# Kernel optimization log

Measured on AMD Instinct MI355X. Metric: run time of the kernel, lower is better.

Reference implementation:

```python
import jax, jax.numpy as jnp
import numpy as np

# --- static config (mirrors init_kwargs) ---
B, N, CBEV = 4, 4, 64
D, FH, FW = 41, 16, 44          # depth bins, feature H/W after downsample
OGH, OGW, DS = 256, 704, 16     # original image dims, downsample
NX, NY, NZ = 240, 240, 1        # BEV grid (x, y, z)
DX = np.array([0.4, 0.4, 20.0], np.float32)            # voxel size
BX = np.array([-47.8, -47.8, 0.0], np.float32)          # voxel grid origin (bound+dx/2)


def _frustum():
    # [D, FH, FW, 3] with (u_pixel, v_pixel, depth); UD discretization 4..44 step 1
    ds = (4.0 + np.arange(D, dtype=np.float32)).reshape(D, 1, 1) * np.ones((1, FH, FW), np.float32)
    xs = np.linspace(0.0, OGW - 1, FW, dtype=np.float32).reshape(1, 1, FW) * np.ones((D, FH, 1), np.float32)
    ys = np.linspace(0.0, OGH - 1, FH, dtype=np.float32).reshape(1, FH, 1) * np.ones((D, 1, FW), np.float32)
    return jnp.asarray(np.stack([xs, ys, ds], axis=-1))


def setup_inputs() -> dict:
    key = jax.random.key(0)
    x = jax.random.normal(key, (B, N, D, FH, FW, CBEV), dtype=jnp.float32)
    # realistic camera rig: 4 cameras at yaw 0/90/180/270 deg, pinhole intrinsics
    intr = np.zeros((N, 3, 3), np.float32)
    rot = np.zeros((N, 3, 3), np.float32)
    tr = np.zeros((N, 3), np.float32)
    cam2ego = np.array([[0, 0, 1], [-1, 0, 0], [0, -1, 0]], np.float32)  # cam z-fwd -> ego x-fwd
    for n in range(N):
        intr[n] = np.array([[500.0, 0.0, OGW / 2.0], [0.0, 500.0, OGH / 2.0], [0.0, 0.0, 1.0]], np.float32)
        yaw = 2.0 * np.pi * n / N
        c, s = np.cos(yaw), np.sin(yaw)
        Rz = np.array([[c, -s, 0], [s, c, 0], [0, 0, 1]], np.float32)
        rot[n] = Rz @ cam2ego
        tr[n] = np.array([1.5 * c, 1.5 * s, 1.6], np.float32)
    rots = jnp.asarray(np.broadcast_to(rot, (B, N, 3, 3)).copy())
    trans = jnp.asarray(np.broadcast_to(tr, (B, N, 3)).copy())
    intrins = jnp.asarray(np.broadcast_to(intr, (B, N, 3, 3)).copy())
    post_rots = jnp.asarray(np.broadcast_to(np.eye(3, dtype=np.float32), (B, N, 3, 3)).copy())
    post_trans = jnp.zeros((B, N, 3), jnp.float32)
    return {"x": x, "rots": rots, "trans": trans, "intrins": intrins,
            "post_rots": post_rots, "post_trans": post_trans}


def reference(x, rots, trans, intrins, post_rots, post_trans):
    # --- get_geometry: frustum pixel/depth points -> ego-frame xyz ---
    frustum = _frustum()                                            # [D,FH,FW,3]
    pts = frustum[None, None] - post_trans[:, :, None, None, None, :]
    pts = jnp.einsum('bnij,bndhwj->bndhwi', jnp.linalg.inv(post_rots), pts)
    pts = jnp.concatenate([pts[..., :2] * pts[..., 2:3], pts[..., 2:3]], axis=-1)
    combine = rots @ jnp.linalg.inv(intrins)
    pts = jnp.einsum('bnij,bndhwj->bndhwi', combine, pts) + trans[:, :, None, None, None, :]
    # --- voxel_pooling: quantize, mask OOB, segment-sum into dense BEV grid ---
    dx = jnp.asarray(DX)
    bx = jnp.asarray(BX)
    vox = ((pts - (bx - dx / 2.0)) / dx).astype(jnp.int32)          # trunc, same as torch .long()
    vx, vy, vz = vox[..., 0], vox[..., 1], vox[..., 2]              # [B,N,D,FH,FW]
    kept = (vx >= 0) & (vx < NX) & (vy >= 0) & (vy < NY) & (vz >= 0) & (vz < NZ)
    bidx = jnp.arange(B, dtype=jnp.int32)[:, None, None, None, None]
    nvox = B * NZ * NY * NX
    lin = bidx * (NZ * NY * NX) + vz * (NY * NX) + vy * NX + vx
    lin = jnp.where(kept, lin, nvox).reshape(-1)                    # invalid -> dummy bin
    feats = x.reshape(-1, CBEV)                                     # [Nprime, C]
    sums = jax.ops.segment_sum(feats, lin, num_segments=nvox + 1)[:nvox]
    final = sums.reshape(B, NZ, NY, NX, CBEV).transpose(0, 1, 4, 2, 3)  # [B,Z,C,Y,X]
    # torch: cat(final.unbind(dim=2), 1) on [B,C,Z,Y,X] -> [B, Z*C, Y, X] z-major
    return final.reshape(B, NZ * CBEV, NY, NX)
```

## Files before the change

### kernel.cpp

```cpp
#include <hip/hip_runtime.h>

#define BB   4
#define NNC  4
#define DDEP 41
#define FHH  16
#define FWW  44
#define CC   64
#define NXX  240
#define NYY  240
#define NVOX (BB*NYY*NXX)
#define NTRI (BB*NNC*DDEP*FWW)
#define SLOTS 8

#define W_CNT  0
#define W_TAB  (NVOX*4)
#define W_VSUM (W_TAB + NVOX*SLOTS*4)

__device__ __forceinline__ void inv3x3_upper_f32(const float K[9], float o[9]) {
    float a00 = __fdiv_rn(1.0f, K[0]);
    float a11 = __fdiv_rn(1.0f, K[4]);
    float a22 = __fdiv_rn(1.0f, K[8]);
    float b01 = __fmul_rn(-a11, __fmul_rn(a00, K[1]));
    float x0 = __fadd_rn(__fmul_rn(a00, K[2]), __fmul_rn(b01, K[5]));
    float x1 = __fmul_rn(a11, K[5]);
    float b02 = __fmul_rn(-a22, x0);
    float b12 = __fmul_rn(-a22, x1);
    o[0]=a00; o[1]=b01; o[2]=b02;
    o[3]=0.0f; o[4]=a11; o[5]=b12;
    o[6]=0.0f; o[7]=0.0f; o[8]=a22;
}

__global__ void __launch_bounds__(256) megageom(
        const float* __restrict__ x,
        const float* __restrict__ rots,
        const float* __restrict__ trans,
        const float* __restrict__ intrins,
        const float* __restrict__ post_rots,
        const float* __restrict__ post_trans,
        int* __restrict__ cnt,
        int* __restrict__ table,
        float* __restrict__ vsum) {
    int tri  = blockIdx.x*4 + (threadIdx.x >> 6);
    int lane = threadIdx.x & 63;
    if (tri >= NTRI) return;

    int w  = tri % FWW;
    int d  = (tri / FWW) % DDEP;
    int bn = tri / (FWW*DDEP);

    float K[9], PR[9], R[9];
    #pragma unroll
    for (int i = 0; i < 9; ++i) {
        K[i]  = intrins[bn*9 + i];
        PR[i] = post_rots[bn*9 + i];
        R[i]  = rots[bn*9 + i];
    }
    float Ki[9], PRi[9];
    inv3x3_upper_f32(K, Ki);
    inv3x3_upper_f32(PR, PRi);
    float C[9];
    #pragma unroll
    for (int i = 0; i < 3; ++i)
        #pragma unroll
        for (int j = 0; j < 3; ++j) {
            float s = __fmul_rn(R[i*3+0], Ki[0*3+j]);
            s = __fadd_rn(s, __fmul_rn(R[i*3+1], Ki[1*3+j]));
            s = __fadd_rn(s, __fmul_rn(R[i*3+2], Ki[2*3+j]));
            C[i*3+j] = s;
        }
    float ptx = post_trans[bn*3+0], pty = post_trans[bn*3+1], ptz = post_trans[bn*3+2];
    float trx = trans[bn*3+0], try_ = trans[bn*3+1], trz = trans[bn*3+2];

    int h = lane & 15;
    float u  = (float)((double)w * (703.0/43.0));
    float v  = (float)((double)h * 17.0);
    float dd = (float)(4 + d);

    float p0x = __fsub_rn(u,  ptx);
    float p0y = __fsub_rn(v,  pty);
    float p0z = __fsub_rn(dd, ptz);
    float p1x = __fadd_rn(__fadd_rn(__fmul_rn(PRi[0],p0x), __fmul_rn(PRi[1],p0y)), __fmul_rn(PRi[2],p0z));
    float p1y = __fadd_rn(__fadd_rn(__fmul_rn(PRi[3],p0x), __fmul_rn(PRi[4],p0y)), __fmul_rn(PRi[5],p0z));
    float p1z = __fadd_rn(__fadd_rn(__fmul_rn(PRi[6],p0x), __fmul_rn(PRi[7],p0y)), __fmul_rn(PRi[8],p0z));
    float p2x = __fmul_rn(p1x, p1z);
    float p2y = __fmul_rn(p1y, p1z);
    float p2z = p1z;
    float ex = __fadd_rn(__fadd_rn(__fmul_rn(C[0],p2x), __fmul_rn(C[1],p2y)), __fmul_rn(C[2],p2z));
    float ey = __fadd_rn(__fadd_rn(__fmul_rn(C[3],p2x), __fmul_rn(C[4],p2y)), __fmul_rn(C[5],p2z));
    float ez = __fadd_rn(__fadd_rn(__fmul_rn(C[6],p2x), __fmul_rn(C[7],p2y)), __fmul_rn(C[8],p2z));
    float gx = __fadd_rn(ex, trx);
    float gy = __fadd_rn(ey, try_);
    float gz = __fadd_rn(ez, trz);

    float qx = __fdiv_rn(__fsub_rn(gx, -48.0f), 0.4f);
    float qy = __fdiv_rn(__fsub_rn(gy, -48.0f), 0.4f);
    float qz = __fdiv_rn(__fsub_rn(gz, -10.0f), 20.0f);
    int vx = (int)qx;
    int vy = (int)qy;
    int vz = (int)qz;

    bool kept = (vx >= 0) & (vx < NXX) & (vy >= 0) & (vy < NYY) & (vz == 0) & (lane < 16);
    unsigned int mask = (unsigned int)(__ballot(kept) & 0xFFFFull);
    if (mask == 0) return;

    const float* xb = x + (size_t)((bn*DDEP + d)*FHH*FWW + w)*CC + lane;
    float a[8];
    #pragma unroll
    for (int k = 0; k < 8; ++k) a[k] = 0.0f;
    #pragma unroll
    for (int hh = 0; hh < 16; ++hh)
        if ((mask >> hh) & 1) a[hh & 7] += xb[(size_t)hh*(FWW*CC)];
    #pragma unroll
    for (int k = 0; k < 4; ++k) a[k] += a[k + 4];
    vsum[(size_t)tri*CC + lane] = (a[0] + a[1]) + (a[2] + a[3]);

    if (lane == 0) {
        int b  = bn / NNC;
        int vb = b*(NYY*NXX) + vy*NXX + vx;
        int sl = atomicAdd(&cnt[vb], 1);
        if (sl < SLOTS) table[vb*SLOTS + sl] = tri;
    }
}

__global__ void __launch_bounds__(256) assemble(
        const int* __restrict__ cnt,
        const int* __restrict__ table,
        const float* __restrict__ vsum,
        float* __restrict__ out) {
    __shared__ float lds[16*65];
    int tid  = threadIdx.x;
    int wid  = tid >> 6;
    int lane = tid & 63;
    int v0   = blockIdx.x*16;

    #pragma unroll
    for (int k = 0; k < 4; ++k) {
        int cell = v0 + wid*4 + k;
        int n = cnt[cell]; if (n > SLOTS) n = SLOTS;
        const int* tp = table + cell*SLOTS;
        int tt = (lane < n) ? tp[lane] : 0;
        float s0 = 0.0f, s1 = 0.0f, s2 = 0.0f, s3 = 0.0f;
        int i = 0;
        for (; i + 4 <= n; i += 4) {
            int t0 = __shfl(tt, i+0), t1 = __shfl(tt, i+1);
            int t2 = __shfl(tt, i+2), t3 = __shfl(tt, i+3);
            s0 += vsum[(size_t)t0*CC + lane];
            s1 += vsum[(size_t)t1*CC + lane];
            s2 += vsum[(size_t)t2*CC + lane];
            s3 += vsum[(size_t)t3*CC + lane];
        }
        for (; i < n; ++i) s0 += vsum[(size_t)__shfl(tt, i)*CC + lane];
        lds[(wid*4 + k)*65 + lane] = (s0 + s1) + (s2 + s3);
    }
    __syncthreads();

    int c = tid >> 2, q = tid & 3;
    float4 f;
    f.x = lds[(q*4 + 0)*65 + c];
    f.y = lds[(q*4 + 1)*65 + c];
    f.z = lds[(q*4 + 2)*65 + c];
    f.w = lds[(q*4 + 3)*65 + c];
    int b  = v0 / (NYY*NXX);
    int yx = v0 % (NYY*NXX);
    *(float4*)&out[(size_t)b*(CC*NYY*NXX) + (size_t)c*(NYY*NXX) + yx + q*4] = f;
}

extern "C" void kernel_launch(void* const* d_in, const int* in_sizes, int n_in,
                              void* d_out, int out_size, void* d_ws, size_t ws_size,
                              hipStream_t stream) {
    const float* x          = (const float*)d_in[0];
    const float* rots       = (const float*)d_in[1];
    const float* trans      = (const float*)d_in[2];
    const float* intrins    = (const float*)d_in[3];
    const float* post_rots  = (const float*)d_in[4];
    const float* post_trans = (const float*)d_in[5];
    float* out = (float*)d_out;

    char* ws = (char*)d_ws;
    int*   cnt   = (int*)(ws + W_CNT);
    int*   table = (int*)(ws + W_TAB);
    float* vsum  = (float*)(ws + W_VSUM);

    hipMemsetAsync(cnt, 0, NVOX*sizeof(int), stream);
    megageom<<<(NTRI + 3)/4, 256, 0, stream>>>(x, rots, trans, intrins,
                                               post_rots, post_trans,
                                               cnt, table, vsum);
    assemble<<<NVOX/16, 256, 0, stream>>>(cnt, table, vsum, out);
}
```

Measured before the change: 243.1 us.

## Defer feature gathering to assemble and pack counters and table entries

The geometry kernel no longer reads features or writes per-triple partial sums. It only records (triple index, 16-bit height mask) entries in the per-cell table, and it packs per-cell counters into bytes so the memset shrinks fourfold. The assemble kernel now gathers the masked x rows directly, which removes the vsum write and reread round trip. Each geometry wavefront now handles four triples at 16 lanes each. In exchange, the feature gathers move into the assemble pass, with data-dependent loops over mask bits, and the byte counters could overflow if more than 255 triples hit one cell.

```diff
diff --git a/kernel.cpp b/kernel.cpp
--- a/kernel.cpp
+++ b/kernel.cpp
@@ -13,8 +13,7 @@
 #define SLOTS 8
 
 #define W_CNT  0
-#define W_TAB  (NVOX*4)
-#define W_VSUM (W_TAB + NVOX*SLOTS*4)
+#define W_TAB  (NVOX)
 
 __device__ __forceinline__ void inv3x3_upper_f32(const float K[9], float o[9]) {
     float a00 = __fdiv_rn(1.0f, K[0]);
@@ -30,23 +29,24 @@
     o[6]=0.0f; o[7]=0.0f; o[8]=a22;
 }
 
-__global__ void __launch_bounds__(256) megageom(
-        const float* __restrict__ x,
+__global__ void __launch_bounds__(256) geom(
         const float* __restrict__ rots,
         const float* __restrict__ trans,
         const float* __restrict__ intrins,
         const float* __restrict__ post_rots,
         const float* __restrict__ post_trans,
-        int* __restrict__ cnt,
-        int* __restrict__ table,
-        float* __restrict__ vsum) {
-    int tri  = blockIdx.x*4 + (threadIdx.x >> 6);
+        unsigned int* __restrict__ cntp,
+        unsigned int* __restrict__ table) {
+    int wid  = threadIdx.x >> 6;
     int lane = threadIdx.x & 63;
-    if (tri >= NTRI) return;
+    int sub  = lane >> 4;
+    int h    = lane & 15;
+    int tri  = (blockIdx.x*4 + wid)*4 + sub;
 
-    int w  = tri % FWW;
-    int d  = (tri / FWW) % DDEP;
-    int bn = tri / (FWW*DDEP);
+    int w    = tri % FWW;
+    int rest = tri / FWW;
+    int d    = rest % DDEP;
+    int bn   = rest / DDEP;
 
     float K[9], PR[9], R[9];
     #pragma unroll
@@ -71,7 +71,6 @@
     float ptx = post_trans[bn*3+0], pty = post_trans[bn*3+1], ptz = post_trans[bn*3+2];
     float trx = trans[bn*3+0], try_ = trans[bn*3+1], trz = trans[bn*3+2];
 
-    int h = lane & 15;
     float u  = (float)((double)w * (703.0/43.0));
     float v  = (float)((double)h * 17.0);
     float dd = (float)(4 + d);
@@ -99,33 +98,24 @@
     int vy = (int)qy;
     int vz = (int)qz;
 
-    bool kept = (vx >= 0) & (vx < NXX) & (vy >= 0) & (vy < NYY) & (vz == 0) & (lane < 16);
-    unsigned int mask = (unsigned int)(__ballot(kept) & 0xFFFFull);
-    if (mask == 0) return;
+    bool kept = (vx >= 0) & (vx < NXX) & (vy >= 0) & (vy < NYY) & (vz == 0);
+    unsigned long long bal = __ballot(kept);
+    unsigned int mask = (unsigned int)((bal >> (sub*16)) & 0xFFFFull);
 
-    const float* xb = x + (size_t)((bn*DDEP + d)*FHH*FWW + w)*CC + lane;
-    float a[8];
-    #pragma unroll
-    for (int k = 0; k < 8; ++k) a[k] = 0.0f;
-    #pragma unroll
-    for (int hh = 0; hh < 16; ++hh)
-        if ((mask >> hh) & 1) a[hh & 7] += xb[(size_t)hh*(FWW*CC)];
-    #pragma unroll
-    for (int k = 0; k < 4; ++k) a[k] += a[k + 4];
-    vsum[(size_t)tri*CC + lane] = (a[0] + a[1]) + (a[2] + a[3]);
-
-    if (lane == 0) {
+    if (h == 0 && mask != 0) {
         int b  = bn / NNC;
         int vb = b*(NYY*NXX) + vy*NXX + vx;
-        int sl = atomicAdd(&cnt[vb], 1);
-        if (sl < SLOTS) table[vb*SLOTS + sl] = tri;
+        unsigned int sh  = 8u*(vb & 3);
+        unsigned int old = atomicAdd(&cntp[vb >> 2], 1u << sh);
+        unsigned int sl  = (old >> sh) & 0xFFu;
+        if (sl < SLOTS) table[vb*SLOTS + sl] = ((unsigned int)tri << 16) | mask;
     }
 }
 
 __global__ void __launch_bounds__(256) assemble(
-        const int* __restrict__ cnt,
-        const int* __restrict__ table,
-        const float* __restrict__ vsum,
+        const float* __restrict__ x,
+        const unsigned int* __restrict__ cntp,
+        const unsigned int* __restrict__ table,
         float* __restrict__ out) {
     __shared__ float lds[16*65];
     int tid  = threadIdx.x;
@@ -133,24 +123,41 @@
     int lane = tid & 63;
     int v0   = blockIdx.x*16;
 
+    unsigned int cw = cntp[(v0 >> 2) + wid];
+
     #pragma unroll
     for (int k = 0; k < 4; ++k) {
         int cell = v0 + wid*4 + k;
-        int n = cnt[cell]; if (n > SLOTS) n = SLOTS;
-        const int* tp = table + cell*SLOTS;
-        int tt = (lane < n) ? tp[lane] : 0;
-        float s0 = 0.0f, s1 = 0.0f, s2 = 0.0f, s3 = 0.0f;
-        int i = 0;
-        for (; i + 4 <= n; i += 4) {
-            int t0 = __shfl(tt, i+0), t1 = __shfl(tt, i+1);
-            int t2 = __shfl(tt, i+2), t3 = __shfl(tt, i+3);
-            s0 += vsum[(size_t)t0*CC + lane];
-            s1 += vsum[(size_t)t1*CC + lane];
-            s2 += vsum[(size_t)t2*CC + lane];
-            s3 += vsum[(size_t)t3*CC + lane];
+        int n = (int)((cw >> (8*k)) & 0xFFu); if (n > SLOTS) n = SLOTS;
+        unsigned int ent = (lane < n) ? table[cell*SLOTS + lane] : 0u;
+        float a[8];
+        #pragma unroll
+        for (int q = 0; q < 8; ++q) a[q] = 0.0f;
+        int j = 0;
+        for (int i = 0; i < n; ++i) {
+            unsigned int e = __shfl((int)ent, i);
+            int tri  = (int)(e >> 16);
+            unsigned int m = e & 0xFFFFu;
+            int w    = tri % FWW;
+            int rest = tri / FWW;
+            int d    = rest % DDEP;
+            int bn   = rest / DDEP;
+            const float* xb = x + (size_t)((bn*DDEP + d)*FHH*FWW + w)*CC + lane;
+            if (m == 0xFFFFu) {
+                #pragma unroll
+                for (int hh = 0; hh < 16; ++hh)
+                    a[hh & 7] += xb[(size_t)hh*(FWW*CC)];
+            } else {
+                while (m) {
+                    int hh = __ffs(m) - 1;
+                    m &= m - 1;
+                    a[(j++) & 7] += xb[(size_t)hh*(FWW*CC)];
+                }
+            }
         }
-        for (; i < n; ++i) s0 += vsum[(size_t)__shfl(tt, i)*CC + lane];
-        lds[(wid*4 + k)*65 + lane] = (s0 + s1) + (s2 + s3);
+        #pragma unroll
+        for (int q = 0; q < 4; ++q) a[q] += a[q + 4];
+        lds[(wid*4 + k)*65 + lane] = (a[0] + a[1]) + (a[2] + a[3]);
     }
     __syncthreads();
 
@@ -177,13 +184,11 @@
     float* out = (float*)d_out;
 
     char* ws = (char*)d_ws;
-    int*   cnt   = (int*)(ws + W_CNT);
-    int*   table = (int*)(ws + W_TAB);
-    float* vsum  = (float*)(ws + W_VSUM);
+    unsigned int* cntp  = (unsigned int*)(ws + W_CNT);
+    unsigned int* table = (unsigned int*)(ws + W_TAB);
 
-    hipMemsetAsync(cnt, 0, NVOX*sizeof(int), stream);
-    megageom<<<(NTRI + 3)/4, 256, 0, stream>>>(x, rots, trans, intrins,
-                                               post_rots, post_trans,
-                                               cnt, table, vsum);
-    assemble<<<NVOX/16, 256, 0, stream>>>(cnt, table, vsum, out);
+    hipMemsetAsync(cntp, 0, NVOX, stream);
+    geom<<<NTRI/16, 256, 0, stream>>>(rots, trans, intrins, post_rots, post_trans,
+                                      cntp, table);
+    assemble<<<NVOX/16, 256, 0, stream>>>(x, cntp, table, out);
 }
```

Result: faster. 235.4 us (-3.2%).
